# Kernel optimization log

Measured on AMD Instinct MI355X. Metric: run time of the kernel, lower is better.

## Reference

```python
import jax, jax.numpy as jnp
import numpy as np

B, N, C, D = 16, 2048, 256, 256


def setup_inputs() -> dict:
    key = jax.random.key(0)
    ks = jax.random.split(key, 8)
    x = jax.random.normal(ks[0], (B, N, C), dtype=jnp.float32)
    valid_len = jax.random.randint(ks[1], (B,), 0, N)
    # nn.Linear params: weight [out, in], bias [out]
    s = 1.0 / np.sqrt(C)
    Wq = jax.random.uniform(ks[2], (D, C), dtype=jnp.float32, minval=-s, maxval=s)
    bq = jax.random.uniform(ks[3], (D,), dtype=jnp.float32, minval=-s, maxval=s)
    Wk = jax.random.uniform(ks[4], (D, C), dtype=jnp.float32, minval=-s, maxval=s)
    bk = jax.random.uniform(ks[5], (D,), dtype=jnp.float32, minval=-s, maxval=s)
    Wv = jax.random.uniform(ks[6], (D, C), dtype=jnp.float32, minval=-s, maxval=s)
    bv = jax.random.uniform(ks[7], (D,), dtype=jnp.float32, minval=-s, maxval=s)
    return {"x": x, "valid_len": valid_len, "Wq": Wq, "bq": bq,
            "Wk": Wk, "bk": bk, "Wv": Wv, "bv": bv}


def reference(x, valid_len, Wq, bq, Wk, bk, Wv, bv):
    # QKV projections (nn.Linear: x @ W^T + b)
    q = jnp.einsum('bnc,dc->bnd', x, Wq) + bq
    k = jnp.einsum('bnc,dc->bnd', x, Wk) + bk
    v = jnp.einsum('bnc,dc->bnd', x, Wv) + bv
    # scores [B, N, N] = q @ k^T (no scaling: scale_factor_d unused in forward)
    scores = jnp.einsum('bnd,bmd->bnm', q, k)
    # key-side valid-length mask: arange(N) < valid_len[b], broadcast over queries
    mask = jnp.arange(N)[None, :] < valid_len[:, None]          # [B, N]
    scores = jnp.where(mask[:, None, :], scores, jnp.float32(-1000000.0))
    attn = jax.nn.softmax(scores, axis=-1)
    return jnp.einsum('bnm,bmd->bnd', attn, v)
```

## Files before the change

### kernel.cpp

```cpp
#include <hip/hip_runtime.h>
#include <hip/hip_bf16.h>
#include <stdint.h>

typedef __attribute__((ext_vector_type(8))) _Float16 half8;
typedef __attribute__((ext_vector_type(4))) _Float16 half4;
typedef __attribute__((ext_vector_type(2))) __fp16 fp16x2;
typedef __attribute__((ext_vector_type(4))) float f32x4;
typedef __attribute__((ext_vector_type(16))) float f32x16;
typedef __attribute__((ext_vector_type(4))) float float4v;

#define DEVI static __device__ __forceinline__

constexpr int Bb = 16, Nn = 2048, Cc = 256, Dd = 256;

DEVI unsigned short f2h_bits(float f) {
  _Float16 h = (_Float16)f;
  union { _Float16 h; unsigned short u; } c;
  c.h = h;
  return c.u;
}

DEVI void gl_lds16(const void* gsrc, void* ldst) {
  __builtin_amdgcn_global_load_lds(
      (const __attribute__((address_space(1))) unsigned int*)gsrc,
      (__attribute__((address_space(3))) unsigned int*)ldst, 16, 0, 0);
}

DEVI f32x4 mfma16h(half8 a, half8 b, f32x4 c) {
  return __builtin_amdgcn_mfma_f32_16x16x32_f16(a, b, c, 0, 0, 0);
}
DEVI f32x16 mfma32h(half8 a, half8 b, f32x16 c) {
  return __builtin_amdgcn_mfma_f32_32x32x16_f16(a, b, c, 0, 0, 0);
}

DEVI unsigned int pkrtz(float a, float b) {
  union { fp16x2 h; unsigned int u; } c;
  c.h = __builtin_amdgcn_cvt_pkrtz(a, b);
  return c.u;
}

__global__ void k_split(const float* __restrict__ x, const float* __restrict__ wq,
                        const float* __restrict__ wk, const float* __restrict__ wv,
                        const int* __restrict__ vlen, _Float16* __restrict__ xh,
                        _Float16* __restrict__ wh, int* __restrict__ sched) {
  __shared__ int ntb[16];
  __shared__ int bofg[16];
  if (blockIdx.x == 8960) {
    int t = threadIdx.x;
    if (t < 16) {
      int L = vlen[t];
      int Lk = (L == 0) ? Nn : L;
      ntb[t] = (Lk + 63) >> 6;
    }
    __syncthreads();
    if (t < 16) {
      int r = 0;
      for (int j = 0; j < 16; ++j)
        if (ntb[j] > ntb[t] || (ntb[j] == ntb[t] && j < t)) ++r;
      int g = (r < 8) ? r : 15 - r;
      int lb = (r < 8) ? 0 : 1;
      bofg[g * 2 + lb] = t;
    }
    __syncthreads();
    for (int s = 0; s < 2; ++s) {
      int ti = s * 256 + t;
      int g = ti >> 6, li = ti & 63;
      int lb = li >> 5, qi = (li >> 1) & 15, kh = li & 1;
      int b = bofg[g * 2 + lb];
      int full = ntb[b];
      int myv = kh ? (full > 16 ? full - 16 : 0) : (full > 16 ? 16 : full);
      int r = 0;
      for (int j = 0; j < 64; ++j) {
        int bj = bofg[g * 2 + (j >> 5)];
        int fj = ntb[bj];
        int vj = (j & 1) ? (fj > 16 ? fj - 16 : 0) : (fj > 16 ? 16 : fj);
        if (vj > myv || (vj == myv && j < li)) ++r;
      }
      sched[g * 64 + r] = b * 32 + qi * 2 + kh;
    }
    return;
  }
  int i = blockIdx.x * 256 + threadIdx.x;
  if (i < 2097152) {
    float4v v = reinterpret_cast<const float4v*>(x)[i];
    half4 h;
#pragma unroll
    for (int j = 0; j < 4; ++j) h[j] = (_Float16)v[j];
    reinterpret_cast<half4*>(xh)[i] = h;
  } else {
    int ii = i - 2097152;
    int mat = ii >> 16;
    int rem = ii & 65535;
    const float* w = (mat == 0) ? wq : ((mat == 1) ? wk : wv);
    wh[(size_t)mat * 65536 + rem] = (_Float16)w[rem];
  }
}

__global__ __launch_bounds__(256, 2) void k_qkv(
    const _Float16* __restrict__ xh, const _Float16* __restrict__ wh,
    const float* __restrict__ bq, const float* __restrict__ bk, const float* __restrict__ bv,
    _Float16* __restrict__ qout, _Float16* __restrict__ kout, _Float16* __restrict__ vt) {
  __shared__ __align__(16) unsigned short smem[17408];

  const int tid = threadIdx.x;
  const int m0 = blockIdx.x * 128;
  const int n0 = blockIdx.y * 128;
  const int mat = blockIdx.z;
  const _Float16* wmat = wh + (size_t)mat * 65536;
  const int wave = tid >> 6, lane = tid & 63;
  const int wr = wave >> 1, wc = wave & 1;
  const int l15 = lane & 15, lq = lane >> 4;

  f32x4 zero4 = {0.f, 0.f, 0.f, 0.f};
  f32x4 acc[4][4];
#pragma unroll
  for (int a = 0; a < 4; ++a)
#pragma unroll
    for (int b2 = 0; b2 < 4; ++b2) acc[a][b2] = zero4;

  char* As = (char*)smem;
  char* Bs = (char*)smem + 16384;

  for (int kc = 0; kc < 4; ++kc) {
#pragma unroll
    for (int i = 0; i < 4; ++i) {
      int p = i * 4096 + tid * 16;
      int row = p >> 7;
      int src_in_row = (p & 127) ^ ((row & 7) << 4);
      const char* g = (const char*)(xh + (size_t)(m0 + row) * Cc + kc * 64) + src_in_row;
      gl_lds16(g, As + p);
    }
#pragma unroll
    for (int i = 0; i < 4; ++i) {
      int p = i * 4096 + tid * 16;
      int row = p >> 7;
      int src_in_row = (p & 127) ^ ((row & 7) << 4);
      const char* g = (const char*)(wmat + (size_t)(n0 + row) * Cc + kc * 64) + src_in_row;
      gl_lds16(g, Bs + p);
    }
    __syncthreads();
#pragma unroll
    for (int ks = 0; ks < 2; ++ks) {
      half8 af[4], bfr[4];
#pragma unroll
      for (int mf = 0; mf < 4; ++mf) {
        int row = wr * 64 + mf * 16 + l15;
        int byte = (row * 128 + ks * 64 + lq * 16) ^ ((row & 7) << 4);
        af[mf] = *(const half8*)(As + byte);
      }
#pragma unroll
      for (int nf = 0; nf < 4; ++nf) {
        int row = wc * 64 + nf * 16 + l15;
        int byte = (row * 128 + ks * 64 + lq * 16) ^ ((row & 7) << 4);
        bfr[nf] = *(const half8*)(Bs + byte);
      }
#pragma unroll
      for (int mf = 0; mf < 4; ++mf)
#pragma unroll
        for (int nf = 0; nf < 4; ++nf) acc[mf][nf] = mfma16h(af[mf], bfr[nf], acc[mf][nf]);
    }
    __syncthreads();
  }

  const float* bias = (mat == 0) ? bq : ((mat == 1) ? bk : bv);
  if (mat < 2) {
    _Float16* oo = (mat == 0) ? qout : kout;
#pragma unroll
    for (int nf = 0; nf < 4; ++nf) {
      int col = n0 + wc * 64 + nf * 16 + l15;
      float bval = bias[col];
#pragma unroll
      for (int mf = 0; mf < 4; ++mf) {
        int grow = m0 + wr * 64 + mf * 16 + lq * 4;
#pragma unroll
        for (int r = 0; r < 4; ++r)
          oo[(size_t)(grow + r) * Dd + col] = (_Float16)(acc[mf][nf][r] + bval);
      }
    }
  } else {
    __syncthreads();
#pragma unroll
    for (int nf = 0; nf < 4; ++nf) {
      int dl = wc * 64 + nf * 16 + l15;
      float bval = bias[n0 + dl];
#pragma unroll
      for (int mf = 0; mf < 4; ++mf) {
        int nl = wr * 64 + mf * 16 + lq * 4;
#pragma unroll
        for (int r = 0; r < 4; ++r) smem[dl * 136 + nl + r] = f2h_bits(acc[mf][nf][r] + bval);
      }
    }
    __syncthreads();
    const int bbat = m0 >> 11, tok0 = m0 & 2047;
#pragma unroll
    for (int pss = 0; pss < 8; ++pss) {
      int idx = pss * 256 + tid;
      int dl = idx >> 4;
      int cu = idx & 15;
      half8 vval = *(const half8*)((const char*)smem + dl * 272 + cu * 16);
      size_t off = ((size_t)bbat * Dd + n0 + dl) * Nn + tok0 + cu * 8;
      *(half8*)(vt + off) = vval;
    }
  }
}

__global__ __launch_bounds__(512, 2) void k_attn_f(
    const _Float16* __restrict__ qg, const _Float16* __restrict__ kin,
    const _Float16* __restrict__ vt, const int* __restrict__ vlen,
    const int* __restrict__ sched, _Float16* __restrict__ Op,
    float* __restrict__ ml) {
  __shared__ __align__(16) char SMEM[149504];
  char* const KVb = SMEM;
  unsigned int* const PL = (unsigned int*)(SMEM + 131072);
  float* const mex = (float*)(SMEM + 147456);
  float* const lex = (float*)(SMEM + 148480);

  const int tid = threadIdx.x;
  const int wave = tid >> 6, lane = tid & 63;
  const int l31 = lane & 31, h = lane >> 5;
  const int wq = wave >> 1, wk = wave & 1;
  const int g = blockIdx.x & 7;
  const int slot = blockIdx.x >> 3;

  for (int s = 0; s < 2; ++s) {
    const int item = sched[g * 64 + (s == 0 ? slot : 63 - slot)];
    const int b = item >> 5;
    const int q0 = ((item >> 1) & 15) * 128;
    const int kh = item & 1;
    const int kst = kh * 1024;
    const int L = vlen[b];
    const bool uni = (L == 0);
    const int Lk = uni ? Nn : L;
    const int avail = Lk - kst;
    int nt = (avail > 0) ? ((avail + 63) >> 6) : 0;
    nt = nt > 16 ? 16 : nt;
    const size_t prow = (size_t)(b * 2 + kh) * Nn + q0;

    if (nt == 0) {
      if (tid < 128) {
        ml[(prow + tid) * 2 + 0] = -1e30f;
        ml[(prow + tid) * 2 + 1] = 0.f;
      }
      continue;
    }

    const char* kbase = (const char*)(kin + (size_t)b * Nn * Dd);
    const char* vbase = (const char*)(vt + (size_t)b * Dd * Nn);
    const char* qbase = (const char*)(qg + ((size_t)b * Nn + q0) * Dd);

    auto STAGE = [&](int buf, int t) {
      char* dst = KVb + buf * 65536;
      const int k0 = kst + t * 64;
#pragma unroll
      for (int i = 0; i < 4; ++i) {
        int p = i * 8192 + tid * 16;
        int row = p >> 9;
        int sl = ((p & 511) >> 4) ^ (row & 31);
        gl_lds16(kbase + (size_t)(k0 + row) * 512 + (sl << 4), dst + p);
      }
#pragma unroll
      for (int i = 0; i < 4; ++i) {
        int p = i * 8192 + tid * 16;
        int r = p >> 9;
        int sl = ((p & 511) >> 4) ^ (r & 31);
        int cl = sl << 4;
        int d = r * 4 + (cl >> 7);
        int kbyte = cl & 127;
        gl_lds16(vbase + (size_t)d * (Nn * 2) + (size_t)k0 * 2 + kbyte, dst + 32768 + p);
      }
    };

    STAGE(0, 0);
#pragma unroll
    for (int i = 0; i < 8; ++i) {
      int p = i * 8192 + tid * 16;
      int row = p >> 9;
      int sl = ((p & 511) >> 4) ^ (row & 31);
      gl_lds16(qbase + (size_t)row * 512 + (sl << 4), KVb + 65536 + p);
    }
    asm volatile("s_waitcnt vmcnt(0)" ::: "memory");
    asm volatile("s_barrier" ::: "memory");

    half8 qreg[16];
    {
      const int row = wq * 32 + l31;
#pragma unroll
      for (int kt = 0; kt < 16; ++kt) {
        int byte = row * 512 + (((kt * 2 + h) ^ (row & 31)) << 4);
        qreg[kt] = *(const half8*)(KVb + 65536 + byte);
      }
    }
    asm volatile("s_waitcnt lgkmcnt(0)" ::: "memory");
    asm volatile("s_barrier" ::: "memory");

    f32x16 acc[4];
#pragma unroll
    for (int dg = 0; dg < 4; ++dg)
#pragma unroll
      for (int r = 0; r < 16; ++r) acc[dg][r] = 0.f;
    float m = -__builtin_inff();
    float lsum = 0.f;

    for (int t = 0; t < nt; ++t) {
      const int cur = t & 1;
      if (t + 1 < nt) {
        STAGE(cur ^ 1, t + 1);
        asm volatile("s_waitcnt vmcnt(8)" ::: "memory");
      } else {
        asm volatile("s_waitcnt vmcnt(0)" ::: "memory");
      }
      asm volatile("s_barrier" ::: "memory");

      const char* Ks = KVb + cur * 65536;
      const char* Vs = Ks + 32768;
      const int k0 = kst + t * 64;

      f32x16 st;
#pragma unroll
      for (int r = 0; r < 16; ++r) st[r] = 0.f;
      if (!uni) {
        const int key = wk * 32 + l31;
        __builtin_amdgcn_s_setprio(1);
#pragma unroll
        for (int kt = 0; kt < 16; ++kt) {
          int byte = key * 512 + (((kt * 2 + h) ^ l31) << 4);
          half8 kf = *(const half8*)(Ks + byte);
          st = mfma32h(kf, qreg[kt], st);
        }
        __builtin_amdgcn_s_setprio(0);
        if (k0 + 64 > L) {
#pragma unroll
          for (int r = 0; r < 16; ++r) {
            int keyg = k0 + wk * 32 + (r & 3) + 8 * (r >> 2) + 4 * h;
            if (keyg >= L) st[r] = -1e6f;
          }
        }
      }

      float pm = st[0];
#pragma unroll
      for (int r = 1; r < 16; ++r) pm = fmaxf(pm, st[r]);
      pm = fmaxf(pm, __shfl_xor(pm, 32));
      if (lane < 32) mex[wave * 32 + lane] = pm;
      asm volatile("s_waitcnt lgkmcnt(0)\ns_barrier" ::: "memory");
      float pmo = mex[(wave ^ 1) * 32 + l31];
      float mnew = fmaxf(m, fmaxf(pm, pmo));
      float scale = __expf(m - mnew);
      m = mnew;
      float psum = 0.f;
#pragma unroll
      for (int r = 0; r < 16; ++r) {
        float p_ = __expf(st[r] - mnew);
        st[r] = p_;
        psum += p_;
      }
      lsum = lsum * scale + psum;

#pragma unroll
      for (int i = 0; i < 8; ++i) {
        unsigned int pk = pkrtz(st[2 * i], st[2 * i + 1]);
        int kp = wk * 16 + 4 * (i >> 1) + (i & 1) + 2 * h;
        PL[wq * 1024 + kp * 32 + l31] = pk;
      }
      asm volatile("s_waitcnt lgkmcnt(0)\ns_barrier" ::: "memory");

      union { unsigned int u[4]; half8 v; } pf0, pf1, pf2, pf3;
#pragma unroll
      for (int w = 0; w < 4; ++w) {
        pf0.u[w] = PL[wq * 1024 + (0 * 8 + h * 4 + w) * 32 + l31];
        pf1.u[w] = PL[wq * 1024 + (1 * 8 + h * 4 + w) * 32 + l31];
        pf2.u[w] = PL[wq * 1024 + (2 * 8 + h * 4 + w) * 32 + l31];
        pf3.u[w] = PL[wq * 1024 + (3 * 8 + h * 4 + w) * 32 + l31];
      }

#pragma unroll
      for (int dg = 0; dg < 4; ++dg)
#pragma unroll
        for (int r = 0; r < 16; ++r) acc[dg][r] *= scale;

      __builtin_amdgcn_s_setprio(1);
#pragma unroll
      for (int dg = 0; dg < 4; ++dg) {
        int r = wk * 32 + dg * 8 + (l31 >> 2);
#pragma unroll
        for (int ks = 0; ks < 4; ++ks) {
          int slotv = (l31 & 3) * 8 + ks * 2 + h;
          half8 vf = *(const half8*)(Vs + r * 512 + ((slotv ^ (r & 31)) << 4));
          acc[dg] = mfma32h(vf, ks == 0 ? pf0.v : (ks == 1 ? pf1.v : (ks == 2 ? pf2.v : pf3.v)),
                            acc[dg]);
        }
      }
      __builtin_amdgcn_s_setprio(0);

      asm volatile("s_barrier" ::: "memory");
    }

    lsum += __shfl_xor(lsum, 32);
    if (lane < 32) lex[wave * 32 + lane] = lsum;
    asm volatile("s_waitcnt lgkmcnt(0)\ns_barrier" ::: "memory");
    float ltot = lsum + lex[(wave ^ 1) * 32 + l31];
    float linv = 1.f / ltot;

    if (h == 0 && wk == 0) {
      size_t qq = prow + wq * 32 + l31;
      ml[qq * 2 + 0] = m;
      ml[qq * 2 + 1] = ltot;
    }

    _Float16* T = (_Float16*)SMEM;
    {
      const int ql = wq * 32 + l31;
#pragma unroll
      for (int dg = 0; dg < 4; ++dg)
#pragma unroll
        for (int r = 0; r < 16; ++r) {
          int d = wk * 128 + dg * 32 + (r & 3) + 8 * (r >> 2) + 4 * h;
          T[ql * 264 + d] = (_Float16)(acc[dg][r] * linv);
        }
    }
    asm volatile("s_waitcnt lgkmcnt(0)\ns_barrier" ::: "memory");

    {
      const int rb = tid >> 6;
      const int c4 = (tid & 63) * 4;
#pragma unroll
      for (int i = 0; i < 16; ++i) {
        int row = rb + i * 8;
        half4 v = *(const half4*)(T + row * 264 + c4);
        *(half4*)(Op + (prow + row) * Dd + c4) = v;
      }
    }
    asm volatile("s_waitcnt lgkmcnt(0)\ns_barrier" ::: "memory");
  }
}

__global__ __launch_bounds__(256) void k_comb(const _Float16* __restrict__ Op,
                                              const float* __restrict__ ml,
                                              float* __restrict__ out) {
  int rid = blockIdx.x * 4 + (threadIdx.x >> 6);
  int lane = threadIdx.x & 63;
  int b = rid >> 11, q = rid & 2047;
  size_t i0 = (size_t)(b * 2 + 0) * Nn + q;
  size_t i1 = (size_t)(b * 2 + 1) * Nn + q;
  float m0 = ml[i0 * 2], l0 = ml[i0 * 2 + 1];
  float m1 = ml[i1 * 2], l1 = ml[i1 * 2 + 1];
  float M = fmaxf(m0, m1);
  float c0 = (l0 > 0.f) ? __expf(m0 - M) * l0 : 0.f;
  float c1 = (l1 > 0.f) ? __expf(m1 - M) * l1 : 0.f;
  float inv = 1.f / (c0 + c1);
  c0 *= inv;
  c1 *= inv;
  float4v o = {0.f, 0.f, 0.f, 0.f};
  if (c0 > 0.f) {
    half4 o0 = *(const half4*)(Op + i0 * 256 + lane * 4);
#pragma unroll
    for (int j = 0; j < 4; ++j) o[j] = c0 * (float)o0[j];
  }
  if (c1 > 0.f) {
    half4 o1 = *(const half4*)(Op + i1 * 256 + lane * 4);
#pragma unroll
    for (int j = 0; j < 4; ++j) o[j] += c1 * (float)o1[j];
  }
  *(float4v*)(out + ((size_t)b * Nn + q) * 256 + lane * 4) = o;
}

__global__ __launch_bounds__(512, 2) void k_attn(
    const _Float16* __restrict__ qg, const _Float16* __restrict__ kin,
    const _Float16* __restrict__ vt, const int* __restrict__ vlen,
    float* __restrict__ out) {
  __shared__ __align__(16) char SMEM[149504];
  char* const KVb = SMEM;
  unsigned int* const PL = (unsigned int*)(SMEM + 131072);
  float* const mex = (float*)(SMEM + 147456);
  float* const lex = (float*)(SMEM + 148480);

  const int tid = threadIdx.x;
  const int wave = tid >> 6, lane = tid & 63;
  const int l31 = lane & 31, h = lane >> 5;
  const int wq = wave >> 1, wk = wave & 1;
  const int id = blockIdx.x;
  const int g = id & 7;
  const int j = id >> 3;
  const int b = g + 8 * (j >> 4);
  const int q0 = (j & 15) * 128;
  const int L = vlen[b];
  const bool uni = (L == 0);
  const int Lk = uni ? Nn : L;
  const int nt = (Lk + 63) >> 6;

  const char* kbase = (const char*)(kin + (size_t)b * Nn * Dd);
  const char* vbase = (const char*)(vt + (size_t)b * Dd * Nn);
  const char* qbase = (const char*)(qg + ((size_t)b * Nn + q0) * Dd);

  auto STAGE = [&](int buf, int t) {
    char* dst = KVb + buf * 65536;
    const int k0 = t * 64;
#pragma unroll
    for (int i = 0; i < 4; ++i) {
      int p = i * 8192 + tid * 16;
      int row = p >> 9;
      int sl = ((p & 511) >> 4) ^ (row & 31);
      gl_lds16(kbase + (size_t)(k0 + row) * 512 + (sl << 4), dst + p);
    }
#pragma unroll
    for (int i = 0; i < 4; ++i) {
      int p = i * 8192 + tid * 16;
      int r = p >> 9;
      int sl = ((p & 511) >> 4) ^ (r & 31);
      int cl = sl << 4;
      int d = r * 4 + (cl >> 7);
      int kbyte = cl & 127;
      gl_lds16(vbase + (size_t)d * (Nn * 2) + (size_t)k0 * 2 + kbyte, dst + 32768 + p);
    }
  };

  STAGE(0, 0);
#pragma unroll
  for (int i = 0; i < 8; ++i) {
    int p = i * 8192 + tid * 16;
    int row = p >> 9;
    int sl = ((p & 511) >> 4) ^ (row & 31);
    gl_lds16(qbase + (size_t)row * 512 + (sl << 4), KVb + 65536 + p);
  }
  asm volatile("s_waitcnt vmcnt(0)" ::: "memory");
  asm volatile("s_barrier" ::: "memory");

  half8 qreg[16];
  {
    const int row = wq * 32 + l31;
#pragma unroll
    for (int kt = 0; kt < 16; ++kt) {
      int byte = row * 512 + (((kt * 2 + h) ^ (row & 31)) << 4);
      qreg[kt] = *(const half8*)(KVb + 65536 + byte);
    }
  }
  asm volatile("s_waitcnt lgkmcnt(0)" ::: "memory");
  asm volatile("s_barrier" ::: "memory");

  f32x16 acc[4];
#pragma unroll
  for (int dg = 0; dg < 4; ++dg)
#pragma unroll
    for (int r = 0; r < 16; ++r) acc[dg][r] = 0.f;
  float m = -__builtin_inff();
  float lsum = 0.f;

  for (int t = 0; t < nt; ++t) {
    const int cur = t & 1;
    if (t + 1 < nt) {
      STAGE(cur ^ 1, t + 1);
      asm volatile("s_waitcnt vmcnt(8)" ::: "memory");
    } else {
      asm volatile("s_waitcnt vmcnt(0)" ::: "memory");
    }
    asm volatile("s_barrier" ::: "memory");

    const char* Ks = KVb + cur * 65536;
    const char* Vs = Ks + 32768;
    const int k0 = t * 64;

    f32x16 st;
#pragma unroll
    for (int r = 0; r < 16; ++r) st[r] = 0.f;
    if (!uni) {
      const int key = wk * 32 + l31;
      __builtin_amdgcn_s_setprio(1);
#pragma unroll
      for (int kt = 0; kt < 16; ++kt) {
        int byte = key * 512 + (((kt * 2 + h) ^ l31) << 4);
        half8 kf = *(const half8*)(Ks + byte);
        st = mfma32h(kf, qreg[kt], st);
      }
      __builtin_amdgcn_s_setprio(0);
      if (k0 + 64 > L) {
#pragma unroll
        for (int r = 0; r < 16; ++r) {
          int keyg = k0 + wk * 32 + (r & 3) + 8 * (r >> 2) + 4 * h;
          if (keyg >= L) st[r] = -1e6f;
        }
      }
    }

    float pm = st[0];
#pragma unroll
    for (int r = 1; r < 16; ++r) pm = fmaxf(pm, st[r]);
    pm = fmaxf(pm, __shfl_xor(pm, 32));
    if (lane < 32) mex[wave * 32 + lane] = pm;
    asm volatile("s_waitcnt lgkmcnt(0)\ns_barrier" ::: "memory");
    float pmo = mex[(wave ^ 1) * 32 + l31];
    float mnew = fmaxf(m, fmaxf(pm, pmo));
    float scale = __expf(m - mnew);
    m = mnew;
    float psum = 0.f;
#pragma unroll
    for (int r = 0; r < 16; ++r) {
      float p_ = __expf(st[r] - mnew);
      st[r] = p_;
      psum += p_;
    }
    lsum = lsum * scale + psum;

#pragma unroll
    for (int i = 0; i < 8; ++i) {
      unsigned int pk = pkrtz(st[2 * i], st[2 * i + 1]);
      int kp = wk * 16 + 4 * (i >> 1) + (i & 1) + 2 * h;
      PL[wq * 1024 + kp * 32 + l31] = pk;
    }
    asm volatile("s_waitcnt lgkmcnt(0)\ns_barrier" ::: "memory");

    union { unsigned int u[4]; half8 v; } pf0, pf1, pf2, pf3;
#pragma unroll
    for (int w = 0; w < 4; ++w) {
      pf0.u[w] = PL[wq * 1024 + (0 * 8 + h * 4 + w) * 32 + l31];
      pf1.u[w] = PL[wq * 1024 + (1 * 8 + h * 4 + w) * 32 + l31];
      pf2.u[w] = PL[wq * 1024 + (2 * 8 + h * 4 + w) * 32 + l31];
      pf3.u[w] = PL[wq * 1024 + (3 * 8 + h * 4 + w) * 32 + l31];
    }

#pragma unroll
    for (int dg = 0; dg < 4; ++dg)
#pragma unroll
      for (int r = 0; r < 16; ++r) acc[dg][r] *= scale;

    __builtin_amdgcn_s_setprio(1);
#pragma unroll
    for (int dg = 0; dg < 4; ++dg) {
      int r = wk * 32 + dg * 8 + (l31 >> 2);
#pragma unroll
      for (int ks = 0; ks < 4; ++ks) {
        int slotv = (l31 & 3) * 8 + ks * 2 + h;
        half8 vf = *(const half8*)(Vs + r * 512 + ((slotv ^ (r & 31)) << 4));
        acc[dg] = mfma32h(vf, ks == 0 ? pf0.v : (ks == 1 ? pf1.v : (ks == 2 ? pf2.v : pf3.v)),
                          acc[dg]);
      }
    }
    __builtin_amdgcn_s_setprio(0);

    asm volatile("s_barrier" ::: "memory");
  }

  lsum += __shfl_xor(lsum, 32);
  if (lane < 32) lex[wave * 32 + lane] = lsum;
  asm volatile("s_waitcnt lgkmcnt(0)\ns_barrier" ::: "memory");
  float linv = 1.f / (lsum + lex[(wave ^ 1) * 32 + l31]);

  float* T = (float*)SMEM;
  {
    const int ql = wq * 32 + l31;
#pragma unroll
    for (int dg = 0; dg < 4; ++dg)
#pragma unroll
      for (int r = 0; r < 16; ++r) {
        int d = wk * 128 + dg * 32 + (r & 3) + 8 * (r >> 2) + 4 * h;
        T[ql * 260 + d] = acc[dg][r] * linv;
      }
  }
  asm volatile("s_waitcnt lgkmcnt(0)\ns_barrier" ::: "memory");

  {
    const int rb = tid >> 6;
    const int c4 = (tid & 63) * 4;
#pragma unroll
    for (int i = 0; i < 16; ++i) {
      int row = rb + i * 8;
      float4v v = *(const float4v*)(T + row * 260 + c4);
      *(float4v*)(out + ((size_t)b * Nn + q0 + row) * Dd + c4) = v;
    }
  }
}

extern "C" void kernel_launch(void* const* d_in, const int* in_sizes, int n_in,
                              void* d_out, int out_size, void* d_ws, size_t ws_size,
                              hipStream_t stream) {
  const float* x = (const float*)d_in[0];
  const int* vlen = (const int*)d_in[1];
  const float* Wq = (const float*)d_in[2];
  const float* bq = (const float*)d_in[3];
  const float* Wk = (const float*)d_in[4];
  const float* bk = (const float*)d_in[5];
  const float* Wv = (const float*)d_in[6];
  const float* bv = (const float*)d_in[7];
  float* out = (float*)d_out;
  char* ws = (char*)d_ws;

  _Float16* qh = (_Float16*)(ws);
  _Float16* kk = (_Float16*)(ws + 16777216);
  _Float16* vt = (_Float16*)(ws + 33554432);
  _Float16* wh = (_Float16*)(ws + 50331648);
  _Float16* Op = (_Float16*)(ws + 51380224);
  float* ml = (float*)(ws + 84934656);
  int* sched = (int*)(ws + 85458944);
  _Float16* xh = (_Float16*)d_out;

  k_split<<<8961, 256, 0, stream>>>(x, Wq, Wk, Wv, vlen, xh, wh, sched);
  k_qkv<<<dim3(256, 2, 3), 256, 0, stream>>>(xh, wh, bq, bk, bv, qh, kk, vt);
  if (ws_size >= 85460992ull) {
    k_attn_f<<<256, 512, 0, stream>>>(qh, kk, vt, vlen, sched, Op, ml);
    k_comb<<<8192, 256, 0, stream>>>(Op, ml, out);
  } else {
    k_attn<<<256, 512, 0, stream>>>(qh, kk, vt, vlen, out);
  }
}
```

Baseline: 132.1 us.

## Skip split for short batches and merge softmax stats with one barrier

After: 126.5 us. 4.3% less time.

```diff
diff --git a/kernel.cpp b/kernel.cpp
--- a/kernel.cpp
+++ b/kernel.cpp
@@ -68,15 +68,19 @@
       int lb = li >> 5, qi = (li >> 1) & 15, kh = li & 1;
       int b = bofg[g * 2 + lb];
       int full = ntb[b];
-      int myv = kh ? (full > 16 ? full - 16 : 0) : (full > 16 ? 16 : full);
+      bool sp = full > 16;
+      bool valid = sp || (kh == 0);
+      int sz = !valid ? -1 : (sp ? (kh ? full - 16 : 16) : full);
       int r = 0;
       for (int j = 0; j < 64; ++j) {
         int bj = bofg[g * 2 + (j >> 5)];
         int fj = ntb[bj];
-        int vj = (j & 1) ? (fj > 16 ? fj - 16 : 0) : (fj > 16 ? 16 : fj);
-        if (vj > myv || (vj == myv && j < li)) ++r;
-      }
-      sched[g * 64 + r] = b * 32 + qi * 2 + kh;
+        bool spj = fj > 16;
+        bool vj = spj || ((j & 1) == 0);
+        int zj = !vj ? -1 : (spj ? ((j & 1) ? fj - 16 : 16) : fj);
+        if (zj > sz || (zj == sz && j < li)) ++r;
+      }
+      sched[g * 64 + r] = valid ? ((b << 6) | (qi << 2) | (kh << 1) | (sp ? 0 : 1)) : -1;
     }
     return;
   }
@@ -208,12 +212,11 @@
     const _Float16* __restrict__ qg, const _Float16* __restrict__ kin,
     const _Float16* __restrict__ vt, const int* __restrict__ vlen,
     const int* __restrict__ sched, _Float16* __restrict__ Op,
-    float* __restrict__ ml) {
+    float* __restrict__ ml, float* __restrict__ out) {
   __shared__ __align__(16) char SMEM[149504];
   char* const KVb = SMEM;
   unsigned int* const PL = (unsigned int*)(SMEM + 131072);
-  float* const mex = (float*)(SMEM + 147456);
-  float* const lex = (float*)(SMEM + 148480);
+  float* const MLX = (float*)(SMEM + 147456);
 
   const int tid = threadIdx.x;
   const int wave = tid >> 6, lane = tid & 63;
@@ -223,26 +226,19 @@
   const int slot = blockIdx.x >> 3;
 
   for (int s = 0; s < 2; ++s) {
-    const int item = sched[g * 64 + (s == 0 ? slot : 63 - slot)];
-    const int b = item >> 5;
-    const int q0 = ((item >> 1) & 15) * 128;
-    const int kh = item & 1;
-    const int kst = kh * 1024;
+    const int iw = sched[g * 64 + (s == 0 ? slot : 63 - slot)];
+    if (iw < 0) continue;
+    const int b = iw >> 6;
+    const int q0 = ((iw >> 2) & 15) * 128;
+    const int kh = (iw >> 1) & 1;
+    const int whole = iw & 1;
     const int L = vlen[b];
     const bool uni = (L == 0);
     const int Lk = uni ? Nn : L;
-    const int avail = Lk - kst;
-    int nt = (avail > 0) ? ((avail + 63) >> 6) : 0;
-    nt = nt > 16 ? 16 : nt;
+    const int full = (Lk + 63) >> 6;
+    const int kst = whole ? 0 : kh * 1024;
+    const int nt = whole ? full : (kh ? full - 16 : 16);
     const size_t prow = (size_t)(b * 2 + kh) * Nn + q0;
-
-    if (nt == 0) {
-      if (tid < 128) {
-        ml[(prow + tid) * 2 + 0] = -1e30f;
-        ml[(prow + tid) * 2 + 1] = 0.f;
-      }
-      continue;
-    }
 
     const char* kbase = (const char*)(kin + (size_t)b * Nn * Dd);
     const char* vbase = (const char*)(vt + (size_t)b * Dd * Nn);
@@ -341,20 +337,14 @@
 #pragma unroll
       for (int r = 1; r < 16; ++r) pm = fmaxf(pm, st[r]);
       pm = fmaxf(pm, __shfl_xor(pm, 32));
-      if (lane < 32) mex[wave * 32 + lane] = pm;
-      asm volatile("s_waitcnt lgkmcnt(0)\ns_barrier" ::: "memory");
-      float pmo = mex[(wave ^ 1) * 32 + l31];
-      float mnew = fmaxf(m, fmaxf(pm, pmo));
-      float scale = __expf(m - mnew);
-      m = mnew;
       float psum = 0.f;
 #pragma unroll
       for (int r = 0; r < 16; ++r) {
-        float p_ = __expf(st[r] - mnew);
+        float p_ = __expf(st[r] - pm);
         st[r] = p_;
         psum += p_;
       }
-      lsum = lsum * scale + psum;
+      psum += __shfl_xor(psum, 32);
 
 #pragma unroll
       for (int i = 0; i < 8; ++i) {
@@ -362,7 +352,21 @@
         int kp = wk * 16 + 4 * (i >> 1) + (i & 1) + 2 * h;
         PL[wq * 1024 + kp * 32 + l31] = pk;
       }
+      if (h == 0) {
+        MLX[(wq * 2 + wk) * 64 + l31] = pm;
+        MLX[(wq * 2 + wk) * 64 + 32 + l31] = psum;
+      }
       asm volatile("s_waitcnt lgkmcnt(0)\ns_barrier" ::: "memory");
+
+      float pm0 = MLX[(wq * 2 + 0) * 64 + l31];
+      float ps0 = MLX[(wq * 2 + 0) * 64 + 32 + l31];
+      float pm1 = MLX[(wq * 2 + 1) * 64 + l31];
+      float ps1 = MLX[(wq * 2 + 1) * 64 + 32 + l31];
+      float mnew = fmaxf(m, fmaxf(pm0, pm1));
+      float scale = __expf(m - mnew);
+      m = mnew;
+      float s0 = __expf(pm0 - mnew), s1 = __expf(pm1 - mnew);
+      lsum = lsum * scale + s0 * ps0 + s1 * ps1;
 
       union { unsigned int u[4]; half8 v; } pf0, pf1, pf2, pf3;
 #pragma unroll
@@ -371,6 +375,15 @@
         pf1.u[w] = PL[wq * 1024 + (1 * 8 + h * 4 + w) * 32 + l31];
         pf2.u[w] = PL[wq * 1024 + (2 * 8 + h * 4 + w) * 32 + l31];
         pf3.u[w] = PL[wq * 1024 + (3 * 8 + h * 4 + w) * 32 + l31];
+      }
+      {
+        _Float16 s0h = (_Float16)s0, s1h = (_Float16)s1;
+        half8 sc0 = {s0h, s0h, s0h, s0h, s0h, s0h, s0h, s0h};
+        half8 sc1 = {s1h, s1h, s1h, s1h, s1h, s1h, s1h, s1h};
+        pf0.v *= sc0;
+        pf1.v *= sc0;
+        pf2.v *= sc1;
+        pf3.v *= sc1;
       }
 
 #pragma unroll
@@ -395,39 +408,61 @@
       asm volatile("s_barrier" ::: "memory");
     }
 
-    lsum += __shfl_xor(lsum, 32);
-    if (lane < 32) lex[wave * 32 + lane] = lsum;
-    asm volatile("s_waitcnt lgkmcnt(0)\ns_barrier" ::: "memory");
-    float ltot = lsum + lex[(wave ^ 1) * 32 + l31];
-    float linv = 1.f / ltot;
-
-    if (h == 0 && wk == 0) {
-      size_t qq = prow + wq * 32 + l31;
-      ml[qq * 2 + 0] = m;
-      ml[qq * 2 + 1] = ltot;
-    }
-
-    _Float16* T = (_Float16*)SMEM;
-    {
-      const int ql = wq * 32 + l31;
-#pragma unroll
-      for (int dg = 0; dg < 4; ++dg)
-#pragma unroll
-        for (int r = 0; r < 16; ++r) {
-          int d = wk * 128 + dg * 32 + (r & 3) + 8 * (r >> 2) + 4 * h;
-          T[ql * 264 + d] = (_Float16)(acc[dg][r] * linv);
+    float linv = 1.f / lsum;
+    if (whole) {
+      if (h == 0 && wk == 0) {
+        size_t qq = (size_t)(b * 2) * Nn + q0 + wq * 32 + l31;
+        ml[qq * 2 + 0] = 1e30f;
+      }
+      float* T = (float*)SMEM;
+      {
+        const int ql = wq * 32 + l31;
+#pragma unroll
+        for (int dg = 0; dg < 4; ++dg)
+#pragma unroll
+          for (int r = 0; r < 16; ++r) {
+            int d = wk * 128 + dg * 32 + (r & 3) + 8 * (r >> 2) + 4 * h;
+            T[ql * 260 + d] = acc[dg][r] * linv;
+          }
+      }
+      asm volatile("s_waitcnt lgkmcnt(0)\ns_barrier" ::: "memory");
+      {
+        const int rb = tid >> 6;
+        const int c4 = (tid & 63) * 4;
+#pragma unroll
+        for (int i = 0; i < 16; ++i) {
+          int row = rb + i * 8;
+          float4v v = *(const float4v*)(T + row * 260 + c4);
+          *(float4v*)(out + ((size_t)b * Nn + q0 + row) * Dd + c4) = v;
         }
-    }
-    asm volatile("s_waitcnt lgkmcnt(0)\ns_barrier" ::: "memory");
-
-    {
-      const int rb = tid >> 6;
-      const int c4 = (tid & 63) * 4;
-#pragma unroll
-      for (int i = 0; i < 16; ++i) {
-        int row = rb + i * 8;
-        half4 v = *(const half4*)(T + row * 264 + c4);
-        *(half4*)(Op + (prow + row) * Dd + c4) = v;
+      }
+    } else {
+      if (h == 0 && wk == 0) {
+        size_t qq = prow + wq * 32 + l31;
+        ml[qq * 2 + 0] = m;
+        ml[qq * 2 + 1] = lsum;
+      }
+      _Float16* T = (_Float16*)SMEM;
+      {
+        const int ql = wq * 32 + l31;
+#pragma unroll
+        for (int dg = 0; dg < 4; ++dg)
+#pragma unroll
+          for (int r = 0; r < 16; ++r) {
+            int d = wk * 128 + dg * 32 + (r & 3) + 8 * (r >> 2) + 4 * h;
+            T[ql * 264 + d] = (_Float16)(acc[dg][r] * linv);
+          }
+      }
+      asm volatile("s_waitcnt lgkmcnt(0)\ns_barrier" ::: "memory");
+      {
+        const int rb = tid >> 6;
+        const int c4 = (tid & 63) * 4;
+#pragma unroll
+        for (int i = 0; i < 16; ++i) {
+          int row = rb + i * 8;
+          half4 v = *(const half4*)(T + row * 264 + c4);
+          *(half4*)(Op + (prow + row) * Dd + c4) = v;
+        }
       }
     }
     asm volatile("s_waitcnt lgkmcnt(0)\ns_barrier" ::: "memory");
@@ -441,8 +476,10 @@
   int lane = threadIdx.x & 63;
   int b = rid >> 11, q = rid & 2047;
   size_t i0 = (size_t)(b * 2 + 0) * Nn + q;
+  float m0 = ml[i0 * 2];
+  if (m0 >= 1e29f) return;
   size_t i1 = (size_t)(b * 2 + 1) * Nn + q;
-  float m0 = ml[i0 * 2], l0 = ml[i0 * 2 + 1];
+  float l0 = ml[i0 * 2 + 1];
   float m1 = ml[i1 * 2], l1 = ml[i1 * 2 + 1];
   float M = fmaxf(m0, m1);
   float c0 = (l0 > 0.f) ? __expf(m0 - M) * l0 : 0.f;
@@ -695,7 +732,7 @@
   k_split<<<8961, 256, 0, stream>>>(x, Wq, Wk, Wv, vlen, xh, wh, sched);
   k_qkv<<<dim3(256, 2, 3), 256, 0, stream>>>(xh, wh, bq, bk, bv, qh, kk, vt);
   if (ws_size >= 85460992ull) {
-    k_attn_f<<<256, 512, 0, stream>>>(qh, kk, vt, vlen, sched, Op, ml);
+    k_attn_f<<<256, 512, 0, stream>>>(qh, kk, vt, vlen, sched, Op, ml, out);
     k_comb<<<8192, 256, 0, stream>>>(Op, ml, out);
   } else {
     k_attn<<<256, 512, 0, stream>>>(qh, kk, vt, vlen, out);
```
